# Performance work log

Measured on AMD Instinct MI355X. Metric: run time of the kernel, lower is better.

The kernel has to match this reference:

```python
import jax, jax.numpy as jnp
import numpy as np

TEMPERATURE = 0.1
EPS = 1e-8  # torch F.cosine_similarity denom clamp


def setup_inputs() -> dict:
    key = jax.random.key(0)
    k1, k2, k3 = jax.random.split(key, 3)
    B, M, D, K = 8, 256, 768, 100
    N = B * M
    transformer_outputs = jax.random.normal(k1, (B, M, D), dtype=jnp.float32)
    cnn_targets = jax.random.normal(k2, (B, M, D), dtype=jnp.float32)
    # uniform sampling with replacement over [0, N) excluding self (multinomial on uniform mask)
    r = jax.random.randint(k3, (N, K), 0, N - 1)
    i = jnp.arange(N)[:, None]
    neg_indices = (r + (r >= i)).astype(jnp.int32)
    return {"transformer_outputs": transformer_outputs, "cnn_targets": cnn_targets, "neg_indices": neg_indices}


def reference(transformer_outputs, cnn_targets, neg_indices):
    B, M, D = transformer_outputs.shape
    N = B * M
    preds = transformer_outputs.reshape(N, D)
    targets = cnn_targets.reshape(N, D)
    pn = preds / jnp.clip(jnp.linalg.norm(preds, axis=-1, keepdims=True), EPS)
    tn = targets / jnp.clip(jnp.linalg.norm(targets, axis=-1, keepdims=True), EPS)
    # all pairwise cosine sims [N, N]; positive on the diagonal, negatives gathered by index
    sim = pn @ tn.T
    pos = jnp.diagonal(sim)                                   # [N]
    neg = sim[jnp.arange(N)[:, None], neg_indices]            # [N, K]
    logits = jnp.concatenate([pos[:, None], neg], axis=1) / TEMPERATURE
    # cross-entropy with label 0 for every row
    loss = -jnp.mean(jax.nn.log_softmax(logits, axis=-1)[:, 0])
    return loss
```

## Files before the change

kernel.cpp:

```cpp
#include <hip/hip_runtime.h>
#include <hip/hip_bf16.h>
#include <math.h>

#define NROWS 2048
#define DDIM  768
#define TNB   384
#define KNEG  100
#define NLOGITS 101
#define MT 7

typedef __attribute__((ext_vector_type(4))) float floatx4;
typedef __attribute__((ext_vector_type(4))) int   intx4;
typedef __attribute__((ext_vector_type(8))) int   intx8;

static constexpr float LFAC = 10.0f / 32.0f;
static constexpr float EPS_NORM = 1e-8f;

__device__ __forceinline__ unsigned pack_fp8x4(float a, float b, float c, float d) {
    int u = 0;
    u = __builtin_amdgcn_cvt_pk_fp8_f32(a, b, u, false);
    u = __builtin_amdgcn_cvt_pk_fp8_f32(c, d, u, true);
    return (unsigned)u;
}

__device__ __forceinline__ unsigned fp4n(float v) {
    const float a = fminf(fabsf(v), 6.0f);
    const unsigned c = (a >= 0.25f) + (a >= 0.75f) + (a >= 1.25f) + (a >= 1.75f)
                     + (a >= 2.5f)  + (a >= 3.5f)  + (a >= 5.0f);
    return c | (v < 0.f ? 8u : 0u);
}

__global__ __launch_bounds__(256) void cl_prep_kernel(
        const float* __restrict__ targets,
        unsigned char* __restrict__ tn4) {
    const int wave = threadIdx.x >> 6, lane = threadIdx.x & 63;
    const int row = blockIdx.x * 4 + wave;
    const float4* tv = (const float4*)(targets + (size_t)row * DDIM);
    const float4 a0 = tv[2 * lane], a1 = tv[2 * lane + 1], b0 = tv[128 + lane];

    float ss = 0.f;
    ss = fmaf(a0.x, a0.x, ss); ss = fmaf(a0.y, a0.y, ss);
    ss = fmaf(a0.z, a0.z, ss); ss = fmaf(a0.w, a0.w, ss);
    ss = fmaf(a1.x, a1.x, ss); ss = fmaf(a1.y, a1.y, ss);
    ss = fmaf(a1.z, a1.z, ss); ss = fmaf(a1.w, a1.w, ss);
    ss = fmaf(b0.x, b0.x, ss); ss = fmaf(b0.y, b0.y, ss);
    ss = fmaf(b0.z, b0.z, ss); ss = fmaf(b0.w, b0.w, ss);
    #pragma unroll
    for (int off = 32; off > 0; off >>= 1) ss += __shfl_xor(ss, off);
    const float sc = 32.0f / fmaxf(sqrtf(ss), EPS_NORM);

    const unsigned ua =  fp4n(a0.x * sc)        | (fp4n(a0.y * sc) << 4)
                      | (fp4n(a0.z * sc) << 8)  | (fp4n(a0.w * sc) << 12)
                      | (fp4n(a1.x * sc) << 16) | (fp4n(a1.y * sc) << 20)
                      | (fp4n(a1.z * sc) << 24) | (fp4n(a1.w * sc) << 28);
    const unsigned short ub = (unsigned short)(fp4n(b0.x * sc)
                      | (fp4n(b0.y * sc) << 4) | (fp4n(b0.z * sc) << 8)
                      | (fp4n(b0.w * sc) << 12));

    __shared__ __align__(16) unsigned char buf[4][TNB];
    *(unsigned*)(&buf[wave][4 * lane]) = ua;
    *(unsigned short*)(&buf[wave][256 + 2 * lane]) = ub;
    __syncthreads();
    if (lane < 24)
        ((uint4*)(tn4 + (size_t)row * TNB))[lane] = *(const uint4*)(&buf[wave][16 * lane]);
}

__global__ __launch_bounds__(256, 5) void cl_rowloss_kernel(
        const float* __restrict__ preds,
        const unsigned char* __restrict__ tn4,
        const int* __restrict__ neg_idx,
        float* __restrict__ row_loss) {
    const int i = blockIdx.x;
    const int tid = threadIdx.x;
    const int wave = tid >> 6, lane = tid & 63;
    const int khalf = wave & 1, thalf = wave >> 1;
    const int q = lane >> 4, rr = lane & 15;

    __shared__ __align__(16) unsigned char Ab[2][32 * TNB];
    __shared__ __align__(16) unsigned char pn8[DDIM];
    __shared__ __align__(16) float parts[2][MT * 16];
    __shared__ int idx_lds[MT * 16];
    __shared__ float sP[3];

    if (tid < MT * 16)
        idx_lds[tid] = (tid == 0 || tid > KNEG) ? i : neg_idx[(size_t)i * KNEG + tid - 1];
    __syncthreads();

    auto stage = [&](int s, int buf, int nchunk) {
        #pragma unroll
        for (int it = 0; it < 3; ++it) {
            const int g = it * 256 + wave * 64 + lane;
            if (g < nchunk) {
                const int rl = g / 24, c = g - rl * 24;
                const int slot = s * 16 + (rl < 16 ? rl : rl + 48);
                const unsigned char* src = tn4 + (size_t)idx_lds[slot] * TNB
                                           + ((c ^ (rl & 7)) << 4);
                __builtin_amdgcn_global_load_lds(
                    (const __attribute__((address_space(1))) void*)src,
                    (__attribute__((address_space(3))) void*)&Ab[buf][(it * 256 + wave * 64) << 4],
                    16, 0, 0);
            }
        }
    };

    float4 pv4;
    if (tid < 192) pv4 = ((const float4*)(preds + (size_t)i * DDIM))[tid];
    stage(0, 0, 768);

    if (tid < 192) {
        float ss = fmaf(pv4.x, pv4.x, fmaf(pv4.y, pv4.y,
                   fmaf(pv4.z, pv4.z, pv4.w * pv4.w)));
        #pragma unroll
        for (int off = 32; off > 0; off >>= 1) ss += __shfl_xor(ss, off);
        if (lane == 0) sP[wave] = ss;
    }
    asm volatile("s_waitcnt lgkmcnt(0)" ::: "memory");
    __builtin_amdgcn_s_barrier();
    __builtin_amdgcn_sched_barrier(0);
    if (tid < 192) {
        const float inv = 1.0f / fmaxf(sqrtf(sP[0] + sP[1] + sP[2]), EPS_NORM);
        ((unsigned*)pn8)[tid] = pack_fp8x4(pv4.x * inv, pv4.y * inv,
                                           pv4.z * inv, pv4.w * inv);
    }
    __syncthreads();

    intx8 b8[3];
    #pragma unroll
    for (int m = 0; m < 3; ++m) {
        const int boff = khalf * 384 + m * 128 + q * 32;
        const intx4 lo = *(const intx4*)(&pn8[boff]);
        const intx4 hi = *(const intx4*)(&pn8[boff + 16]);
        b8[m] = (intx8){lo.x, lo.y, lo.z, lo.w, hi.x, hi.y, hi.z, hi.w};
    }

    floatx4 acc[4] = {};
    const int rbase = (thalf * 16 + rr) * TNB;
    const int rx = rr & 7;

#define CL_S(S, NC_NEXT, DO_STAGE)                                            \
    {                                                                         \
        if (DO_STAGE) stage((S) + 1, ((S) + 1) & 1, NC_NEXT);                 \
        if (!thalf || (S) < 3) {                                              \
            _Pragma("unroll")                                                 \
            for (int m = 0; m < 3; ++m) {                                     \
                const int cl = khalf * 12 + m * 4 + q;                        \
                const intx4 a4 = *(const intx4*)(&Ab[(S) & 1][rbase + ((cl ^ rx) << 4)]); \
                const intx8 a8 = (intx8){a4.x, a4.y, a4.z, a4.w, 0, 0, 0, 0}; \
                acc[S] = __builtin_amdgcn_mfma_scale_f32_16x16x128_f8f6f4(    \
                    a8, b8[m], acc[S], 4 , 0 ,              \
                    0, 127, 0, 127);                                          \
            }                                                                 \
        }                                                                     \
        __syncthreads();                                                      \
    }

    CL_S(0, 768, 1)
    CL_S(1, 768, 1)
    CL_S(2, 384, 1)
    CL_S(3, 0, 0)
#undef CL_S

    if (rr == 0) {
        const int rb = q * 4;
        if (!thalf) {
            #pragma unroll
            for (int t = 0; t < 4; ++t)
                *(floatx4*)(&parts[khalf][t * 16 + rb]) = acc[t];
        } else {
            #pragma unroll
            for (int t = 0; t < 3; ++t)
                *(floatx4*)(&parts[khalf][(t + 4) * 16 + rb]) = acc[t];
        }
    }
    __syncthreads();

    if (wave == 0) {
        const float v0 = (parts[0][lane] + parts[1][lane]) * LFAC;
        float v1 = -INFINITY;
        if (lane <= NLOGITS - 65)
            v1 = (parts[0][64 + lane] + parts[1][64 + lane]) * LFAC;
        const float l0 = __shfl(v0, 0);
        float m = fmaxf(v0, v1);
        #pragma unroll
        for (int off = 32; off > 0; off >>= 1) m = fmaxf(m, __shfl_xor(m, off));
        float e = expf(v0 - m);
        if (lane <= NLOGITS - 65) e += expf(v1 - m);
        #pragma unroll
        for (int off = 32; off > 0; off >>= 1) e += __shfl_xor(e, off);
        if (lane == 0) row_loss[i] = (m + logf(e)) - l0;
    }
}

__global__ void cl_reduce_kernel(const float* __restrict__ row_loss,
                                 float* __restrict__ out) {
    const int tid = threadIdx.x;
    float s = 0.f;
    #pragma unroll
    for (int c = 0; c < 2; ++c) {
        const float4 v = ((const float4*)row_loss)[tid + 256 * c];
        s += (v.x + v.y) + (v.z + v.w);
    }
    #pragma unroll
    for (int off = 32; off > 0; off >>= 1) s += __shfl_down(s, off);
    __shared__ float sw[4];
    const int wave = tid >> 6, lane = tid & 63;
    if (lane == 0) sw[wave] = s;
    __syncthreads();
    if (tid == 0) out[0] = (sw[0] + sw[1] + sw[2] + sw[3]) / (float)NROWS;
}

extern "C" void kernel_launch(void* const* d_in, const int* in_sizes, int n_in,
                              void* d_out, int out_size, void* d_ws, size_t ws_size,
                              hipStream_t stream) {
    const float* preds   = (const float*)d_in[0];
    const float* targets = (const float*)d_in[1];
    const int*   neg_idx = (const int*)d_in[2];
    float* out = (float*)d_out;

    unsigned char* tn4 = (unsigned char*)d_ws;
    float* row_loss = (float*)((char*)d_ws + (size_t)NROWS * TNB);

    cl_prep_kernel<<<NROWS / 4, 256, 0, stream>>>(targets, tn4);
    cl_rowloss_kernel<<<NROWS, 256, 0, stream>>>(preds, tn4, neg_idx, row_loss);
    cl_reduce_kernel<<<1, 256, 0, stream>>>(row_loss, out);
}
```

Before: 21.16 us.

## Prefetch all gather stages up front into four LDS buffers

Replaces the double-buffered, stage-by-stage gather of negative target rows with a single up-front issue of all four stages into four separate LDS buffers. Each compute stage then waits with a decreasing vmcnt count and a raw s_barrier instead of a full __syncthreads. The goal is to put all global-to-LDS loads in flight at once and cut per-stage latency and barrier overhead. The cost is double the LDS footprint, with launch bounds lowered to 3 blocks per CU, and some wasted loads in the last stage.

New measurement: 23.45 us. +10.8%, slower.

```diff
diff --git a/kernel.cpp b/kernel.cpp
--- a/kernel.cpp
+++ b/kernel.cpp
@@ -65,7 +65,7 @@
         ((uint4*)(tn4 + (size_t)row * TNB))[lane] = *(const uint4*)(&buf[wave][16 * lane]);
 }
 
-__global__ __launch_bounds__(256, 5) void cl_rowloss_kernel(
+__global__ __launch_bounds__(256, 3) void cl_rowloss_kernel(
         const float* __restrict__ preds,
         const unsigned char* __restrict__ tn4,
         const int* __restrict__ neg_idx,
@@ -76,7 +76,7 @@
     const int khalf = wave & 1, thalf = wave >> 1;
     const int q = lane >> 4, rr = lane & 15;
 
-    __shared__ __align__(16) unsigned char Ab[2][32 * TNB];
+    __shared__ __align__(16) unsigned char Ab[4][32 * TNB];
     __shared__ __align__(16) unsigned char pn8[DDIM];
     __shared__ __align__(16) float parts[2][MT * 16];
     __shared__ int idx_lds[MT * 16];
@@ -86,18 +86,19 @@
         idx_lds[tid] = (tid == 0 || tid > KNEG) ? i : neg_idx[(size_t)i * KNEG + tid - 1];
     __syncthreads();
 
-    auto stage = [&](int s, int buf, int nchunk) {
+    auto stage = [&](int s, int nchunk) {
         #pragma unroll
         for (int it = 0; it < 3; ++it) {
             const int g = it * 256 + wave * 64 + lane;
             if (g < nchunk) {
                 const int rl = g / 24, c = g - rl * 24;
-                const int slot = s * 16 + (rl < 16 ? rl : rl + 48);
+                const int slot = (rl < 16) ? s * 16 + rl
+                                 : (s < 3 ? s * 16 + rl + 48 : 0);
                 const unsigned char* src = tn4 + (size_t)idx_lds[slot] * TNB
                                            + ((c ^ (rl & 7)) << 4);
                 __builtin_amdgcn_global_load_lds(
                     (const __attribute__((address_space(1))) void*)src,
-                    (__attribute__((address_space(3))) void*)&Ab[buf][(it * 256 + wave * 64) << 4],
+                    (__attribute__((address_space(3))) void*)&Ab[s][(it * 256 + wave * 64) << 4],
                     16, 0, 0);
             }
         }
@@ -105,7 +106,11 @@
 
     float4 pv4;
     if (tid < 192) pv4 = ((const float4*)(preds + (size_t)i * DDIM))[tid];
-    stage(0, 0, 768);
+
+    stage(0, 768);
+    stage(1, 768);
+    stage(2, 768);
+    stage(3, 512);
 
     if (tid < 192) {
         float ss = fmaf(pv4.x, pv4.x, fmaf(pv4.y, pv4.y,
@@ -122,7 +127,9 @@
         ((unsigned*)pn8)[tid] = pack_fp8x4(pv4.x * inv, pv4.y * inv,
                                            pv4.z * inv, pv4.w * inv);
     }
-    __syncthreads();
+    asm volatile("s_waitcnt lgkmcnt(0)" ::: "memory");
+    __builtin_amdgcn_s_barrier();
+    __builtin_amdgcn_sched_barrier(0);
 
     intx8 b8[3];
     #pragma unroll
@@ -137,27 +144,28 @@
     const int rbase = (thalf * 16 + rr) * TNB;
     const int rx = rr & 7;
 
-#define CL_S(S, NC_NEXT, DO_STAGE)                                            \
+#define CL_S(S, NWAIT)                                                        \
     {                                                                         \
-        if (DO_STAGE) stage((S) + 1, ((S) + 1) & 1, NC_NEXT);                 \
+        asm volatile("s_waitcnt vmcnt(" #NWAIT ")" ::: "memory");             \
+        __builtin_amdgcn_s_barrier();                                         \
+        __builtin_amdgcn_sched_barrier(0);                                    \
         if (!thalf || (S) < 3) {                                              \
             _Pragma("unroll")                                                 \
             for (int m = 0; m < 3; ++m) {                                     \
                 const int cl = khalf * 12 + m * 4 + q;                        \
-                const intx4 a4 = *(const intx4*)(&Ab[(S) & 1][rbase + ((cl ^ rx) << 4)]); \
+                const intx4 a4 = *(const intx4*)(&Ab[S][rbase + ((cl ^ rx) << 4)]); \
                 const intx8 a8 = (intx8){a4.x, a4.y, a4.z, a4.w, 0, 0, 0, 0}; \
                 acc[S] = __builtin_amdgcn_mfma_scale_f32_16x16x128_f8f6f4(    \
                     a8, b8[m], acc[S], 4 , 0 ,              \
                     0, 127, 0, 127);                                          \
             }                                                                 \
         }                                                                     \
-        __syncthreads();                                                      \
-    }
-
-    CL_S(0, 768, 1)
-    CL_S(1, 768, 1)
-    CL_S(2, 384, 1)
-    CL_S(3, 0, 0)
+    }
+
+    CL_S(0, 8)
+    CL_S(1, 5)
+    CL_S(2, 2)
+    CL_S(3, 0)
 #undef CL_S
 
     if (rr == 0) {
```
